# Optimization experiments

Measured on AMD Instinct MI355X. Metric: run time of the kernel, lower is better.

The kernel has to match this reference:

```python
import jax, jax.numpy as jnp
import numpy as np

INPUT_DIM = 32
HIDDEN_DIM = 64
OUTPUT_DIM = 16
B = 2_097_152


def _xavier(key, fan_in, fan_out):
    limit = float(np.sqrt(6.0 / (fan_in + fan_out)))
    return jax.random.uniform(key, (fan_in, fan_out), jnp.float32, -limit, limit)


def setup_inputs() -> dict:
    key = jax.random.key(0)
    ks = jax.random.split(key, 5)
    feat = jax.random.normal(ks[0], (B, INPUT_DIM), jnp.float32)
    W0 = _xavier(ks[1], INPUT_DIM, HIDDEN_DIM)
    b0 = jnp.zeros((HIDDEN_DIM,), jnp.float32)
    W1 = _xavier(ks[2], HIDDEN_DIM, HIDDEN_DIM)
    b1 = jnp.zeros((HIDDEN_DIM,), jnp.float32)
    Ws = _xavier(ks[3], HIDDEN_DIM, 1)
    bs = jnp.zeros((1,), jnp.float32)
    Wr = _xavier(ks[4], HIDDEN_DIM, OUTPUT_DIM)
    br = jnp.zeros((OUTPUT_DIM,), jnp.float32)
    return {"feat": feat, "W0": W0, "b0": b0, "W1": W1, "b1": b1,
            "Ws": Ws, "bs": bs, "Wr": Wr, "br": br}


def reference(feat, W0, b0, W1, b1, Ws, bs, Wr, br):
    # hidden MLP: Linear -> ReLU, twice (num_layers=2)
    x = jax.nn.relu(feat @ W0 + b0)          # [B, 64]
    x = jax.nn.relu(x @ W1 + b1)             # [B, 64]
    sigma = (x @ Ws + bs)[:, 0]               # [B]
    sigma = jax.nn.softplus(sigma - 1.0)      # density, shifted softplus
    rgb_feat = x @ Wr + br                    # [B, 16]
    return sigma, rgb_feat
```

## Files before the change

kernel.cpp:

```cpp
#include <hip/hip_runtime.h>
#include <hip/hip_bf16.h>
#include <math.h>

typedef __bf16 bf16_t;
typedef __bf16 bf16x8 __attribute__((ext_vector_type(8)));
typedef float  f32x4  __attribute__((ext_vector_type(4)));

#define WPB 4


__device__ __forceinline__ void pin8(bf16x8& x) {
    f32x4 t = __builtin_bit_cast(f32x4, x);
    asm volatile("" : "+v"(t));
    x = __builtin_bit_cast(bf16x8, t);
}
__device__ __forceinline__ void pin4(f32x4& x) { asm volatile("" : "+v"(x)); }

__device__ __forceinline__ bf16x8 cvt8(f32x4 lo, f32x4 hi) {
    bf16x8 r;
    #pragma unroll
    for (int j = 0; j < 4; ++j) { r[j] = (bf16_t)lo[j]; r[4 + j] = (bf16_t)hi[j]; }
    return r;
}

__device__ __forceinline__ bf16x8 relu_pack(const f32x4 a, const f32x4 b) {
    bf16x8 r;
    #pragma unroll
    for (int j = 0; j < 4; ++j) {
        r[j]     = (bf16_t)fmaxf(a[j], 0.0f);
        r[4 + j] = (bf16_t)fmaxf(b[j], 0.0f);
    }
    return r;
}

__global__ __launch_bounds__(256, 3)
void ngp_mlp_kernel(const float* __restrict__ feat,
                    const float* __restrict__ W0,
                    const float* __restrict__ b0,
                    const float* __restrict__ W1,
                    const float* __restrict__ b1,
                    const float* __restrict__ Ws,
                    const float* __restrict__ bs,
                    const float* __restrict__ Wr,
                    const float* __restrict__ br,
                    float* __restrict__ out_sigma,
                    float* __restrict__ out_rgb,
                    int num_tiles, int wave_stride)
{
    const int tid  = threadIdx.x;
    const int wid  = tid >> 6;
    const int lane = tid & 63;
    const int n    = lane & 15;
    const int q    = lane >> 4;

    bf16x8 w0f[4];
    #pragma unroll
    for (int t = 0; t < 4; ++t)
        #pragma unroll
        for (int j = 0; j < 8; ++j)
            w0f[t][j] = (bf16_t)W0[(8*q + j)*64 + 16*t + n];

    bf16x8 w1f[4][2];
    #pragma unroll
    for (int t = 0; t < 4; ++t)
        #pragma unroll
        for (int c = 0; c < 2; ++c)
            #pragma unroll
            for (int j = 0; j < 8; ++j) {
                const int ch = 16*(2*c + (j >> 2)) + 4*q + (j & 3);
                w1f[t][c][j] = (bf16_t)W1[ch*64 + 16*t + n];
            }

    bf16x8 whf[2][2];
    #pragma unroll
    for (int c = 0; c < 2; ++c)
        #pragma unroll
        for (int j = 0; j < 8; ++j) {
            const int ch = 16*(2*c + (j >> 2)) + 4*q + (j & 3);
            whf[0][c][j] = (bf16_t)Wr[ch*16 + n];
            whf[1][c][j] = (n == 0) ? (bf16_t)Ws[ch] : (bf16_t)0.0f;
        }

    f32x4 b0q[4], b1q[4];
    #pragma unroll
    for (int t = 0; t < 4; ++t) {
        b0q[t] = *(const f32x4*)(b0 + 16*t + 4*q);
        b1q[t] = *(const f32x4*)(b1 + 16*t + 4*q);
    }
    f32x4 brq = *(const f32x4*)(br + 4*q);
    f32x4 sIn = (f32x4){ (q == 0) ? (bs[0] - 1.0f) : 0.0f, 0.0f, 0.0f, 0.0f };

    #pragma unroll
    for (int t = 0; t < 4; ++t) pin8(w0f[t]);
    #pragma unroll
    for (int t = 0; t < 4; ++t)
        #pragma unroll
        for (int c = 0; c < 2; ++c) pin8(w1f[t][c]);
    #pragma unroll
    for (int h = 0; h < 2; ++h)
        #pragma unroll
        for (int c = 0; c < 2; ++c) pin8(whf[h][c]);
    #pragma unroll
    for (int t = 0; t < 4; ++t) { pin4(b0q[t]); pin4(b1q[t]); }
    pin4(brq); pin4(sIn);

    int tile = blockIdx.x * WPB + wid;
    if (tile >= num_tiles) return;

    const float* fp = feat + (size_t)(tile*16 + n)*32 + 8*q;
    f32x4 aLo = __builtin_nontemporal_load((const f32x4*)fp);
    f32x4 aHi = __builtin_nontemporal_load((const f32x4*)fp + 1);

    while (true) {
        const int  nxt  = tile + wave_stride;
        const bool more = (nxt < num_tiles);
        const int  pf   = more ? nxt : tile;
        const float* fpn = feat + (size_t)(pf*16 + n)*32 + 8*q;
        f32x4 aLoN = __builtin_nontemporal_load((const f32x4*)fpn);
        f32x4 aHiN = __builtin_nontemporal_load((const f32x4*)fpn + 1);

        const int rowbase = tile * 16;
        bf16x8 a0 = cvt8(aLo, aHi);

        f32x4 acc0[4];
        #pragma unroll
        for (int t = 0; t < 4; ++t)
            acc0[t] = __builtin_amdgcn_mfma_f32_16x16x32_bf16(w0f[t], a0, b0q[t], 0, 0, 0);

        bf16x8 a1[2];
        a1[0] = relu_pack(acc0[0], acc0[1]);
        a1[1] = relu_pack(acc0[2], acc0[3]);

        f32x4 acc1[4];
        #pragma unroll
        for (int t = 0; t < 4; ++t) {
            acc1[t] = __builtin_amdgcn_mfma_f32_16x16x32_bf16(w1f[t][0], a1[0], b1q[t], 0, 0, 0);
            acc1[t] = __builtin_amdgcn_mfma_f32_16x16x32_bf16(w1f[t][1], a1[1], acc1[t], 0, 0, 0);
        }

        bf16x8 ah[2];
        ah[0] = relu_pack(acc1[0], acc1[1]);
        ah[1] = relu_pack(acc1[2], acc1[3]);

        f32x4 aR = __builtin_amdgcn_mfma_f32_16x16x32_bf16(whf[0][0], ah[0], brq, 0, 0, 0);
        aR       = __builtin_amdgcn_mfma_f32_16x16x32_bf16(whf[0][1], ah[1], aR,  0, 0, 0);
        f32x4 aS = __builtin_amdgcn_mfma_f32_16x16x32_bf16(whf[1][0], ah[0], sIn, 0, 0, 0);
        aS       = __builtin_amdgcn_mfma_f32_16x16x32_bf16(whf[1][1], ah[1], aS,  0, 0, 0);

        __builtin_nontemporal_store(aR, (f32x4*)(out_rgb + ((size_t)rowbase + n) * 16 + 4*q));

        if (q == 0) {
            float z = aS[0];
            float sp = fmaxf(z, 0.0f) + log1pf(expf(-fabsf(z)));
            __builtin_nontemporal_store(sp, out_sigma + rowbase + n);
        }

        if (!more) break;
        tile = nxt;
        aLo  = aLoN;
        aHi  = aHiN;
    }
}

extern "C" void kernel_launch(void* const* d_in, const int* in_sizes, int n_in,
                              void* d_out, int out_size, void* d_ws, size_t ws_size,
                              hipStream_t stream) {
    const float* feat = (const float*)d_in[0];
    const float* W0   = (const float*)d_in[1];
    const float* b0   = (const float*)d_in[2];
    const float* W1   = (const float*)d_in[3];
    const float* b1   = (const float*)d_in[4];
    const float* Ws   = (const float*)d_in[5];
    const float* bs   = (const float*)d_in[6];
    const float* Wr   = (const float*)d_in[7];
    const float* br   = (const float*)d_in[8];

    const int B         = in_sizes[0] / 32;
    const int num_tiles = B / 16;

    float* out_sigma = (float*)d_out;
    float* out_rgb   = out_sigma + B;

    const int blocks = 768;
    ngp_mlp_kernel<<<blocks, 256, 0, stream>>>(feat, W0, b0, W1, b1, Ws, bs, Wr, br,
                                               out_sigma, out_rgb,
                                               num_tiles, blocks * WPB);
}
```

Baseline: 419.3 us.

## Process two row tiles per wave iteration with two-deep prefetch

Each wave now handles a pair of 16-row tiles per loop iteration, interleaving the MFMA chains of the two tiles so their dependencies overlap. It also prefetches input two iterations ahead instead of one, which keeps more loads in flight. Softplus moves to exp2/log2 builtins, and the launch changes to 512 blocks with a lower occupancy hint. The cost is higher register pressure and fewer resident waves.

```diff
diff --git a/kernel.cpp b/kernel.cpp
--- a/kernel.cpp
+++ b/kernel.cpp
@@ -33,7 +33,7 @@
     return r;
 }
 
-__global__ __launch_bounds__(256, 3)
+__global__ __launch_bounds__(256, 2)
 void ngp_mlp_kernel(const float* __restrict__ feat,
                     const float* __restrict__ W0,
                     const float* __restrict__ b0,
@@ -45,7 +45,7 @@
                     const float* __restrict__ br,
                     float* __restrict__ out_sigma,
                     float* __restrict__ out_rgb,
-                    int num_tiles, int wave_stride)
+                    int num_pairs, int wave_stride)
 {
     const int tid  = threadIdx.x;
     const int wid  = tid >> 6;
@@ -104,61 +104,92 @@
     for (int t = 0; t < 4; ++t) { pin4(b0q[t]); pin4(b1q[t]); }
     pin4(brq); pin4(sIn);
 
-    int tile = blockIdx.x * WPB + wid;
-    if (tile >= num_tiles) return;
-
-    const float* fp = feat + (size_t)(tile*16 + n)*32 + 8*q;
-    f32x4 aLo = __builtin_nontemporal_load((const f32x4*)fp);
-    f32x4 aHi = __builtin_nontemporal_load((const f32x4*)fp + 1);
+    int p = blockIdx.x * WPB + wid;
+    if (p >= num_pairs) return;
+    const int W = wave_stride;
+
+    const float* fpc = feat + ((size_t)p*32 + n)*32 + 8*q;
+    f32x4 cAlo = __builtin_nontemporal_load((const f32x4*)fpc);
+    f32x4 cAhi = __builtin_nontemporal_load((const f32x4*)fpc + 1);
+    f32x4 cBlo = __builtin_nontemporal_load((const f32x4*)(fpc + 512));
+    f32x4 cBhi = __builtin_nontemporal_load((const f32x4*)(fpc + 512) + 1);
+
+    const int p1 = (p + W < num_pairs) ? p + W : p;
+    const float* fp1 = feat + ((size_t)p1*32 + n)*32 + 8*q;
+    f32x4 nAlo = __builtin_nontemporal_load((const f32x4*)fp1);
+    f32x4 nAhi = __builtin_nontemporal_load((const f32x4*)fp1 + 1);
+    f32x4 nBlo = __builtin_nontemporal_load((const f32x4*)(fp1 + 512));
+    f32x4 nBhi = __builtin_nontemporal_load((const f32x4*)(fp1 + 512) + 1);
 
     while (true) {
-        const int  nxt  = tile + wave_stride;
-        const bool more = (nxt < num_tiles);
-        const int  pf   = more ? nxt : tile;
-        const float* fpn = feat + (size_t)(pf*16 + n)*32 + 8*q;
-        f32x4 aLoN = __builtin_nontemporal_load((const f32x4*)fpn);
-        f32x4 aHiN = __builtin_nontemporal_load((const f32x4*)fpn + 1);
-
-        const int rowbase = tile * 16;
-        bf16x8 a0 = cvt8(aLo, aHi);
-
-        f32x4 acc0[4];
-        #pragma unroll
-        for (int t = 0; t < 4; ++t)
-            acc0[t] = __builtin_amdgcn_mfma_f32_16x16x32_bf16(w0f[t], a0, b0q[t], 0, 0, 0);
-
-        bf16x8 a1[2];
-        a1[0] = relu_pack(acc0[0], acc0[1]);
-        a1[1] = relu_pack(acc0[2], acc0[3]);
-
-        f32x4 acc1[4];
+        const int  p2 = p + 2*W;
+        const int  pf = (p2 < num_pairs) ? p2 : p;
+        const float* fpn = feat + ((size_t)pf*32 + n)*32 + 8*q;
+        f32x4 mAlo = __builtin_nontemporal_load((const f32x4*)fpn);
+        f32x4 mAhi = __builtin_nontemporal_load((const f32x4*)fpn + 1);
+        f32x4 mBlo = __builtin_nontemporal_load((const f32x4*)(fpn + 512));
+        f32x4 mBhi = __builtin_nontemporal_load((const f32x4*)(fpn + 512) + 1);
+
+        const int rowA = p * 32;
+        const int rowB = rowA + 16;
+        bf16x8 a0A = cvt8(cAlo, cAhi);
+        bf16x8 a0B = cvt8(cBlo, cBhi);
+
+        f32x4 acc0A[4], acc0B[4];
         #pragma unroll
         for (int t = 0; t < 4; ++t) {
-            acc1[t] = __builtin_amdgcn_mfma_f32_16x16x32_bf16(w1f[t][0], a1[0], b1q[t], 0, 0, 0);
-            acc1[t] = __builtin_amdgcn_mfma_f32_16x16x32_bf16(w1f[t][1], a1[1], acc1[t], 0, 0, 0);
-        }
-
-        bf16x8 ah[2];
-        ah[0] = relu_pack(acc1[0], acc1[1]);
-        ah[1] = relu_pack(acc1[2], acc1[3]);
-
-        f32x4 aR = __builtin_amdgcn_mfma_f32_16x16x32_bf16(whf[0][0], ah[0], brq, 0, 0, 0);
-        aR       = __builtin_amdgcn_mfma_f32_16x16x32_bf16(whf[0][1], ah[1], aR,  0, 0, 0);
-        f32x4 aS = __builtin_amdgcn_mfma_f32_16x16x32_bf16(whf[1][0], ah[0], sIn, 0, 0, 0);
-        aS       = __builtin_amdgcn_mfma_f32_16x16x32_bf16(whf[1][1], ah[1], aS,  0, 0, 0);
-
-        __builtin_nontemporal_store(aR, (f32x4*)(out_rgb + ((size_t)rowbase + n) * 16 + 4*q));
+            acc0A[t] = __builtin_amdgcn_mfma_f32_16x16x32_bf16(w0f[t], a0A, b0q[t], 0, 0, 0);
+            acc0B[t] = __builtin_amdgcn_mfma_f32_16x16x32_bf16(w0f[t], a0B, b0q[t], 0, 0, 0);
+        }
+
+        bf16x8 a1A[2], a1B[2];
+        a1A[0] = relu_pack(acc0A[0], acc0A[1]);
+        a1B[0] = relu_pack(acc0B[0], acc0B[1]);
+        a1A[1] = relu_pack(acc0A[2], acc0A[3]);
+        a1B[1] = relu_pack(acc0B[2], acc0B[3]);
+
+        f32x4 acc1A[4], acc1B[4];
+        #pragma unroll
+        for (int t = 0; t < 4; ++t) {
+            acc1A[t] = __builtin_amdgcn_mfma_f32_16x16x32_bf16(w1f[t][0], a1A[0], b1q[t], 0, 0, 0);
+            acc1B[t] = __builtin_amdgcn_mfma_f32_16x16x32_bf16(w1f[t][0], a1B[0], b1q[t], 0, 0, 0);
+            acc1A[t] = __builtin_amdgcn_mfma_f32_16x16x32_bf16(w1f[t][1], a1A[1], acc1A[t], 0, 0, 0);
+            acc1B[t] = __builtin_amdgcn_mfma_f32_16x16x32_bf16(w1f[t][1], a1B[1], acc1B[t], 0, 0, 0);
+        }
+
+        bf16x8 ahA[2], ahB[2];
+        ahA[0] = relu_pack(acc1A[0], acc1A[1]);
+        ahB[0] = relu_pack(acc1B[0], acc1B[1]);
+        ahA[1] = relu_pack(acc1A[2], acc1A[3]);
+        ahB[1] = relu_pack(acc1B[2], acc1B[3]);
+
+        f32x4 aRA = __builtin_amdgcn_mfma_f32_16x16x32_bf16(whf[0][0], ahA[0], brq, 0, 0, 0);
+        f32x4 aRB = __builtin_amdgcn_mfma_f32_16x16x32_bf16(whf[0][0], ahB[0], brq, 0, 0, 0);
+        aRA       = __builtin_amdgcn_mfma_f32_16x16x32_bf16(whf[0][1], ahA[1], aRA, 0, 0, 0);
+        aRB       = __builtin_amdgcn_mfma_f32_16x16x32_bf16(whf[0][1], ahB[1], aRB, 0, 0, 0);
+        f32x4 aSA = __builtin_amdgcn_mfma_f32_16x16x32_bf16(whf[1][0], ahA[0], sIn, 0, 0, 0);
+        f32x4 aSB = __builtin_amdgcn_mfma_f32_16x16x32_bf16(whf[1][0], ahB[0], sIn, 0, 0, 0);
+        aSA       = __builtin_amdgcn_mfma_f32_16x16x32_bf16(whf[1][1], ahA[1], aSA, 0, 0, 0);
+        aSB       = __builtin_amdgcn_mfma_f32_16x16x32_bf16(whf[1][1], ahB[1], aSB, 0, 0, 0);
+
+        __builtin_nontemporal_store(aRA, (f32x4*)(out_rgb + ((size_t)rowA + n) * 16 + 4*q));
+        __builtin_nontemporal_store(aRB, (f32x4*)(out_rgb + ((size_t)rowB + n) * 16 + 4*q));
 
         if (q == 0) {
-            float z = aS[0];
-            float sp = fmaxf(z, 0.0f) + log1pf(expf(-fabsf(z)));
-            __builtin_nontemporal_store(sp, out_sigma + rowbase + n);
-        }
-
-        if (!more) break;
-        tile = nxt;
-        aLo  = aLoN;
-        aHi  = aHiN;
+            float zA  = aSA[0];
+            float eA  = __builtin_exp2f(-fabsf(zA) * 1.44269504f);
+            float spA = fmaxf(zA, 0.0f) + __builtin_log2f(1.0f + eA) * 0.69314718f;
+            __builtin_nontemporal_store(spA, out_sigma + rowA + n);
+            float zB  = aSB[0];
+            float eB  = __builtin_exp2f(-fabsf(zB) * 1.44269504f);
+            float spB = fmaxf(zB, 0.0f) + __builtin_log2f(1.0f + eB) * 0.69314718f;
+            __builtin_nontemporal_store(spB, out_sigma + rowB + n);
+        }
+
+        if (p + W >= num_pairs) break;
+        p += W;
+        cAlo = nAlo; cAhi = nAhi; cBlo = nBlo; cBhi = nBhi;
+        nAlo = mAlo; nAhi = mAhi; nBlo = mBlo; nBhi = mBhi;
     }
 }
 
@@ -176,13 +207,13 @@
     const float* br   = (const float*)d_in[8];
 
     const int B         = in_sizes[0] / 32;
-    const int num_tiles = B / 16;
+    const int num_pairs = B / 32;
 
     float* out_sigma = (float*)d_out;
     float* out_rgb   = out_sigma + B;
 
-    const int blocks = 768;
+    const int blocks = 512;
     ngp_mlp_kernel<<<blocks, 256, 0, stream>>>(feat, W0, b0, W1, b1, Ws, bs, Wr, br,
                                                out_sigma, out_rgb,
-                                               num_tiles, blocks * WPB);
-}
+                                               num_pairs, blocks * WPB);
+}
```

After: 405.1 us. 1.04x faster.
